# Optimization experiments

Measured on AMD Instinct MI355X. Metric: run time of the kernel, lower is better.

The kernel has to match this reference:

```python
import jax, jax.numpy as jnp
import numpy as np

D_MODEL = 512
N_HEADS = 8
HEAD_DIM = 64
INNER = N_HEADS * HEAD_DIM
PAD = 128  # flash-attention style tile padding used by the custom kernel


def setup_inputs() -> dict:
    key = jax.random.key(0)
    ks = jax.random.split(key, 5)
    B, S = 2, 2048
    scale = 0.02
    return {
        "hidden_states": jax.random.normal(ks[0], (B, S, D_MODEL), dtype=jnp.float32),
        "Wq": jax.random.normal(ks[1], (D_MODEL, INNER), dtype=jnp.float32) * scale,
        "Wk": jax.random.normal(ks[2], (D_MODEL, INNER), dtype=jnp.float32) * scale,
        "Wv": jax.random.normal(ks[3], (D_MODEL, INNER), dtype=jnp.float32) * scale,
        "Wo": jax.random.normal(ks[4], (INNER, D_MODEL), dtype=jnp.float32) * scale,
    }


def _padded_attention(q, k, v):
    """Emulates torch.ops.knl.fwd: pad seq to a multiple of PAD, run
    non-causal scaled dot-product attention masking padded keys, then
    slice back to the original length. q,k,v: [B, S, INNER]."""
    B, S, _ = q.shape
    pad_len = (-S) % PAD
    Sp = S + pad_len
    pad_cfg = ((0, 0), (0, pad_len), (0, 0))
    qp = jnp.pad(q, pad_cfg)
    kp = jnp.pad(k, pad_cfg)
    vp = jnp.pad(v, pad_cfg)
    # [B, H, Sp, hd]
    qh = qp.reshape(B, Sp, N_HEADS, HEAD_DIM).transpose(0, 2, 1, 3)
    kh = kp.reshape(B, Sp, N_HEADS, HEAD_DIM).transpose(0, 2, 1, 3)
    vh = vp.reshape(B, Sp, N_HEADS, HEAD_DIM).transpose(0, 2, 1, 3)
    scale = 1.0 / np.sqrt(HEAD_DIM).astype(np.float32)
    scores = jnp.einsum("bhqd,bhkd->bhqk", qh, kh) * scale  # [B,H,Sp,Sp]
    key_valid = jnp.arange(Sp) < S  # mask out padded keys
    scores = jnp.where(key_valid[None, None, None, :], scores, jnp.float32(-1e30))
    probs = jax.nn.softmax(scores, axis=-1)
    out = jnp.einsum("bhqk,bhkd->bhqd", probs, vh)  # [B,H,Sp,hd]
    out = out.transpose(0, 2, 1, 3).reshape(B, Sp, INNER)
    return out[:, :S, :]


def reference(hidden_states, Wq, Wk, Wv, Wo):
    q = hidden_states @ Wq
    k = hidden_states @ Wk
    v = hidden_states @ Wv
    attn = _padded_attention(q, k, v)
    return attn @ Wo
```

## Files before the change

kernel.cpp:

```cpp
#include <hip/hip_runtime.h>

using bf16 = __bf16;
using bf16x4 = __attribute__((ext_vector_type(4))) __bf16;
using bf16x8 = __attribute__((ext_vector_type(8))) __bf16;
using floatx4 = __attribute__((ext_vector_type(4))) float;
using half4 = __attribute__((ext_vector_type(4))) _Float16;
using half8 = __attribute__((ext_vector_type(8))) _Float16;

#define D_MODEL 512
#define S_LEN 2048
#define HD 64
#define NH 8
#define M_TOT 4096
#define NSPLIT 4
#define KSPAN (S_LEN / NSPLIT)
#define QSCALE 0.18033688f

__device__ __forceinline__ bf16x8 ld8(const bf16* p) {
    return *reinterpret_cast<const bf16x8*>(p);
}
__device__ __forceinline__ void gl_lds16(const bf16* g, bf16* l) {
    __builtin_amdgcn_global_load_lds(
        (const __attribute__((address_space(1))) void*)g,
        (__attribute__((address_space(3))) void*)l, 16, 0, 0);
}

__global__ __launch_bounds__(256) void prep(const float* __restrict__ w0,
                                            const float* __restrict__ w1,
                                            const float* __restrict__ w2,
                                            const float* __restrict__ w3,
                                            const float* __restrict__ X,
                                            bf16* __restrict__ WT,
                                            bf16* __restrict__ Xb) {
    int z = blockIdx.z;
    if (z == 4) {
        int i = (blockIdx.x * 256 + threadIdx.x) * 8;
        float4 a = *reinterpret_cast<const float4*>(X + i);
        float4 b = *reinterpret_cast<const float4*>(X + i + 4);
        bf16x8 o;
        o[0] = (bf16)a.x; o[1] = (bf16)a.y; o[2] = (bf16)a.z; o[3] = (bf16)a.w;
        o[4] = (bf16)b.x; o[5] = (bf16)b.y; o[6] = (bf16)b.z; o[7] = (bf16)b.w;
        *reinterpret_cast<bf16x8*>(Xb + i) = o;
        return;
    }
    if (blockIdx.x >= 256) return;
    __shared__ float t[32][33];
    const float* in = z == 0 ? w0 : z == 1 ? w1 : z == 2 ? w2 : w3;
    bf16* o = WT + (size_t)z * D_MODEL * D_MODEL;
    int x = threadIdx.x & 31;
    int y = threadIdx.x >> 5;
    int k0 = (blockIdx.x & 15) * 32, n0 = (blockIdx.x >> 4) * 32;
    for (int r = y; r < 32; r += 8) t[r][x] = in[(size_t)(k0 + r) * D_MODEL + n0 + x];
    __syncthreads();
    for (int r = y; r < 32; r += 8) o[(size_t)(n0 + r) * D_MODEL + k0 + x] = (bf16)t[x][r];
}

__global__ __launch_bounds__(256) void gemm_qkvf(const bf16* __restrict__ X,
                                                 const bf16* __restrict__ WT,
                                                 bf16* __restrict__ qk,
                                                 bf16* __restrict__ VT) {
    __shared__ __align__(16) bf16 As[2][64 * 64];
    __shared__ __align__(16) bf16 Bs[2][64 * 64];
    int lane = threadIdx.x & 63, wave = threadIdx.x >> 6;
    int l15 = lane & 15, quad = lane >> 4;
    int m0 = blockIdx.x * 64;
    int n0 = blockIdx.y * 64;
    int z = n0 >> 9;
    int h = (n0 >> 6) & 7;
    int wm = (wave & 1) * 32, wn = (wave >> 1) * 32;
    float oscale = (z == 0) ? QSCALE : 1.0f;

    int sr = lane >> 3;
    int sc = (lane & 7) ^ sr;
    const bf16* gA = X  + (size_t)(m0 + wave * 16 + sr) * D_MODEL + sc * 8;
    const bf16* gB = WT + (size_t)(n0 + wave * 16 + sr) * D_MODEL + sc * 8;
    int ldsOff = (wave * 16) * 64;
    int rx = l15 & 7;

    gl_lds16(gA, &As[0][ldsOff]);
    gl_lds16(gA + (size_t)8 * D_MODEL, &As[0][ldsOff + 8 * 64]);
    gl_lds16(gB, &Bs[0][ldsOff]);
    gl_lds16(gB + (size_t)8 * D_MODEL, &Bs[0][ldsOff + 8 * 64]);
    __syncthreads();

    floatx4 acc[2][2] = {};
    int cur = 0;
    for (int k0 = 0; k0 < D_MODEL; k0 += 64) {
        if (k0 + 64 < D_MODEL) {
            gl_lds16(gA + k0 + 64, &As[cur ^ 1][ldsOff]);
            gl_lds16(gA + (size_t)8 * D_MODEL + k0 + 64, &As[cur ^ 1][ldsOff + 8 * 64]);
            gl_lds16(gB + k0 + 64, &Bs[cur ^ 1][ldsOff]);
            gl_lds16(gB + (size_t)8 * D_MODEL + k0 + 64, &Bs[cur ^ 1][ldsOff + 8 * 64]);
        }
        bf16x8 af[2][2], bfr[2][2];
        #pragma unroll
        for (int mt = 0; mt < 2; mt++)
            #pragma unroll
            for (int kh = 0; kh < 2; kh++)
                af[mt][kh] = ld8(&As[cur][(wm + mt * 16 + l15) * 64 + (((quad + 4 * kh) ^ rx)) * 8]);
        #pragma unroll
        for (int nt = 0; nt < 2; nt++)
            #pragma unroll
            for (int kh = 0; kh < 2; kh++)
                bfr[nt][kh] = ld8(&Bs[cur][(wn + nt * 16 + l15) * 64 + (((quad + 4 * kh) ^ rx)) * 8]);
        #pragma unroll
        for (int mt = 0; mt < 2; mt++)
            #pragma unroll
            for (int nt = 0; nt < 2; nt++) {
                acc[mt][nt] = __builtin_amdgcn_mfma_f32_16x16x32_bf16(af[mt][0], bfr[nt][0], acc[mt][nt], 0, 0, 0);
                acc[mt][nt] = __builtin_amdgcn_mfma_f32_16x16x32_bf16(af[mt][1], bfr[nt][1], acc[mt][nt], 0, 0, 0);
            }
        __syncthreads();
        cur ^= 1;
    }

    if (z < 2) {
        bf16* dst = qk + (size_t)z * M_TOT * HD * NH;
        #pragma unroll
        for (int mt = 0; mt < 2; mt++)
            #pragma unroll
            for (int nt = 0; nt < 2; nt++)
                #pragma unroll
                for (int r = 0; r < 4; r++) {
                    int m = m0 + wm + mt * 16 + quad * 4 + r;
                    int n = wn + nt * 16 + l15;
                    int b = m >> 11, s = m & 2047;
                    dst[((size_t)(b * NH + h) * S_LEN + s) * HD + n] = (bf16)(acc[mt][nt][r] * oscale);
                }
    } else {
        #pragma unroll
        for (int mt = 0; mt < 2; mt++)
            #pragma unroll
            for (int nt = 0; nt < 2; nt++) {
                int m = m0 + wm + mt * 16 + quad * 4;
                int d = wn + nt * 16 + l15;
                int b = m >> 11, s = m & 2047;
                bf16x4 pk;
                pk[0] = (bf16)acc[mt][nt][0]; pk[1] = (bf16)acc[mt][nt][1];
                pk[2] = (bf16)acc[mt][nt][2]; pk[3] = (bf16)acc[mt][nt][3];
                *reinterpret_cast<bf16x4*>(&VT[((size_t)(b * NH + h) * HD + d) * S_LEN + s]) = pk;
            }
    }
}

__global__ __launch_bounds__(256, 4) void attn_split(const bf16* __restrict__ qg,
                                                     const bf16* __restrict__ kg,
                                                     const bf16* __restrict__ vt,
                                                     _Float16* __restrict__ Opart,
                                                     float* __restrict__ lsum) {
    __shared__ __align__(16) bf16 Kl[2][64 * 64];
    __shared__ __align__(16) bf16 Vl[2][64 * 64];
    int tid = threadIdx.x;
    int lane = tid & 63, wave = tid >> 6;
    int l15 = lane & 15, quad = lane >> 4;
    int bh = blockIdx.y, split = blockIdx.z;
    int q0 = blockIdx.x * 128;
    const bf16* qb = qg + (size_t)bh * S_LEN * HD;
    const bf16* kb = kg + (size_t)bh * S_LEN * HD + (size_t)split * KSPAN * HD;
    const bf16* vb = vt + (size_t)bh * HD * S_LEN + split * KSPAN;
    int qA = q0 + wave * 32 + l15;
    int qB = qA + 16;
    bf16x8 qf[2][2];
    qf[0][0] = ld8(qb + (size_t)qA * HD + quad * 8);
    qf[0][1] = ld8(qb + (size_t)qA * HD + 32 + quad * 8);
    qf[1][0] = ld8(qb + (size_t)qB * HD + quad * 8);
    qf[1][1] = ld8(qb + (size_t)qB * HD + 32 + quad * 8);
    floatx4 O[2][4] = {};
    float l_i[2] = {0.f, 0.f};

    int sr = lane >> 3;
    int sc = (lane & 7) ^ sr;
    const bf16* gK = kb + (size_t)(wave * 16 + sr) * HD + sc * 8;
    const bf16* gV = vb + (size_t)(wave * 16 + sr) * S_LEN + sc * 8;
    int ldsOff = (wave * 16) * 64;
    int rx = l15 & 7;
    int sa = ((quad & 1) << 5) + l15;
    int sb = sa + 16;
    bool himux = (quad & 2) != 0;

    gl_lds16(gK, &Kl[0][ldsOff]);
    gl_lds16(gK + (size_t)8 * HD, &Kl[0][ldsOff + 8 * 64]);
    gl_lds16(gV, &Vl[0][ldsOff]);
    gl_lds16(gV + (size_t)8 * S_LEN, &Vl[0][ldsOff + 8 * 64]);
    __syncthreads();

    int cur = 0;
    for (int kt = 0; kt < KSPAN; kt += 64) {
        if (kt + 64 < KSPAN) {
            gl_lds16(gK + (size_t)(kt + 64) * HD, &Kl[cur ^ 1][ldsOff]);
            gl_lds16(gK + (size_t)(kt + 72) * HD, &Kl[cur ^ 1][ldsOff + 8 * 64]);
            gl_lds16(gV + kt + 64, &Vl[cur ^ 1][ldsOff]);
            gl_lds16(gV + (size_t)8 * S_LEN + kt + 64, &Vl[cur ^ 1][ldsOff + 8 * 64]);
        }

        floatx4 sc4[2][4];
        #pragma unroll
        for (int nt = 0; nt < 4; nt++) {
            bf16x8 a0 = ld8(&Kl[cur][(nt * 16 + l15) * 64 + (quad ^ rx) * 8]);
            bf16x8 a1 = ld8(&Kl[cur][(nt * 16 + l15) * 64 + ((quad + 4) ^ rx) * 8]);
            #pragma unroll
            for (int s = 0; s < 2; s++) {
                floatx4 z = {};
                z = __builtin_amdgcn_mfma_f32_16x16x32_bf16(a0, qf[s][0], z, 0, 0, 0);
                z = __builtin_amdgcn_mfma_f32_16x16x32_bf16(a1, qf[s][1], z, 0, 0, 0);
                sc4[s][nt] = z;
            }
        }

        bf16x8 pb[2][2];
        #pragma unroll
        for (int s = 0; s < 2; s++) {
            int2 pq[4];
            #pragma unroll
            for (int nt = 0; nt < 4; nt++) {
                bf16x4 pk;
                #pragma unroll
                for (int r = 0; r < 4; r++) {
                    float p = exp2f(sc4[s][nt][r]);
                    l_i[s] += p;
                    pk[r] = (bf16)p;
                }
                pq[nt] = __builtin_bit_cast(int2, pk);
            }
            #pragma unroll
            for (int h2 = 0; h2 < 2; h2++) {
                int t0 = __shfl(pq[2 * h2].x,     sa, 64);
                int t1 = __shfl(pq[2 * h2].y,     sa, 64);
                int t2 = __shfl(pq[2 * h2 + 1].x, sa, 64);
                int t3 = __shfl(pq[2 * h2 + 1].y, sa, 64);
                int u0 = __shfl(pq[2 * h2].x,     sb, 64);
                int u1 = __shfl(pq[2 * h2].y,     sb, 64);
                int u2 = __shfl(pq[2 * h2 + 1].x, sb, 64);
                int u3 = __shfl(pq[2 * h2 + 1].y, sb, 64);
                int4 v;
                v.x = himux ? t2 : t0;
                v.y = himux ? t3 : t1;
                v.z = himux ? u2 : u0;
                v.w = himux ? u3 : u1;
                pb[s][h2] = __builtin_bit_cast(bf16x8, v);
            }
        }

        #pragma unroll
        for (int nt = 0; nt < 4; nt++) {
            bf16x8 v0 = ld8(&Vl[cur][(nt * 16 + l15) * 64 + (quad ^ rx) * 8]);
            bf16x8 v1 = ld8(&Vl[cur][(nt * 16 + l15) * 64 + ((quad + 4) ^ rx) * 8]);
            #pragma unroll
            for (int s = 0; s < 2; s++) {
                O[s][nt] = __builtin_amdgcn_mfma_f32_16x16x32_bf16(v0, pb[s][0], O[s][nt], 0, 0, 0);
                O[s][nt] = __builtin_amdgcn_mfma_f32_16x16x32_bf16(v1, pb[s][1], O[s][nt], 0, 0, 0);
            }
        }

        __syncthreads();
        cur ^= 1;
    }

    #pragma unroll
    for (int s = 0; s < 2; s++) {
        l_i[s] += __shfl_xor(l_i[s], 16, 64);
        l_i[s] += __shfl_xor(l_i[s], 32, 64);
        int q = (s == 0) ? qA : qB;
        size_t obase = (((size_t)(split * 16 + bh)) * S_LEN + q) * HD;
        #pragma unroll
        for (int nt = 0; nt < 4; nt++) {
            half4 hv;
            hv[0] = (_Float16)O[s][nt][0]; hv[1] = (_Float16)O[s][nt][1];
            hv[2] = (_Float16)O[s][nt][2]; hv[3] = (_Float16)O[s][nt][3];
            *reinterpret_cast<half4*>(&Opart[obase + nt * 16 + quad * 4]) = hv;
        }
        if (quad == 0)
            lsum[((size_t)(split * 16 + bh)) * S_LEN + q] = l_i[s];
    }
}

__global__ __launch_bounds__(256) void gemm_outm(const _Float16* __restrict__ Opart,
                                                 const float* __restrict__ lsum,
                                                 const bf16* __restrict__ WoT,
                                                 float* __restrict__ out) {
    __shared__ __align__(16) bf16 As[64 * 64];
    __shared__ __align__(16) bf16 Bs[64 * 64];
    __shared__ float invl[64 * 8];
    int tid = threadIdx.x;
    int lane = tid & 63, wave = tid >> 6;
    int l15 = lane & 15, quad = lane >> 4;
    int m0 = blockIdx.x * 64;
    int n0 = blockIdx.y * 64;
    int wm = (wave & 1) * 32, wn = (wave >> 1) * 32;

    for (int i = tid; i < 512; i += 256) {
        int row = i >> 3, h = i & 7;
        int mm = m0 + row;
        int b = mm >> 11, q = mm & 2047;
        float l = 0.f;
        #pragma unroll
        for (int s = 0; s < NSPLIT; s++)
            l += lsum[((size_t)(s * 16 + b * NH + h)) * S_LEN + q];
        invl[i] = 1.f / l;
    }

    int sr = lane >> 3;
    int sc = (lane & 7) ^ sr;
    const bf16* gB = WoT + (size_t)(n0 + wave * 16 + sr) * D_MODEL + sc * 8;
    bf16* ldsA = &As[(wave * 16) * 64];
    bf16* ldsB = &Bs[(wave * 16) * 64];
    int rx = l15 & 7;

    floatx4 acc[2][2] = {};
    for (int k0 = 0; k0 < D_MODEL; k0 += 64) {
        __syncthreads();
        gl_lds16(gB + k0, ldsB);
        gl_lds16(gB + (size_t)8 * D_MODEL + k0, ldsB + 8 * 64);
        int h = k0 >> 6;
        #pragma unroll
        for (int st = 0; st < 2; st++) {
            int row = wave * 16 + sr + st * 8;
            int mm = m0 + row;
            int b = mm >> 11, q = mm & 2047;
            float iv = invl[row * 8 + h];
            float a8[8] = {};
            #pragma unroll
            for (int s = 0; s < NSPLIT; s++) {
                half8 hp = *reinterpret_cast<const half8*>(
                    &Opart[(((size_t)(s * 16 + b * NH + h)) * S_LEN + q) * HD + sc * 8]);
                #pragma unroll
                for (int j = 0; j < 8; j++) a8[j] += (float)hp[j];
            }
            bf16x8 v;
            #pragma unroll
            for (int j = 0; j < 8; j++) v[j] = (bf16)(a8[j] * iv);
            *reinterpret_cast<bf16x8*>(ldsA + st * 512 + lane * 8) = v;
        }
        __syncthreads();
        bf16x8 af[2][2], bfr[2][2];
        #pragma unroll
        for (int mt = 0; mt < 2; mt++)
            #pragma unroll
            for (int kh = 0; kh < 2; kh++)
                af[mt][kh] = ld8(&As[(wm + mt * 16 + l15) * 64 + (((quad + 4 * kh) ^ rx)) * 8]);
        #pragma unroll
        for (int nt = 0; nt < 2; nt++)
            #pragma unroll
            for (int kh = 0; kh < 2; kh++)
                bfr[nt][kh] = ld8(&Bs[(wn + nt * 16 + l15) * 64 + (((quad + 4 * kh) ^ rx)) * 8]);
        #pragma unroll
        for (int mt = 0; mt < 2; mt++)
            #pragma unroll
            for (int nt = 0; nt < 2; nt++) {
                acc[mt][nt] = __builtin_amdgcn_mfma_f32_16x16x32_bf16(af[mt][0], bfr[nt][0], acc[mt][nt], 0, 0, 0);
                acc[mt][nt] = __builtin_amdgcn_mfma_f32_16x16x32_bf16(af[mt][1], bfr[nt][1], acc[mt][nt], 0, 0, 0);
            }
    }

    #pragma unroll
    for (int mt = 0; mt < 2; mt++)
        #pragma unroll
        for (int nt = 0; nt < 2; nt++)
            #pragma unroll
            for (int r = 0; r < 4; r++) {
                int m = m0 + wm + mt * 16 + quad * 4 + r;
                int n = n0 + wn + nt * 16 + l15;
                out[(size_t)m * D_MODEL + n] = acc[mt][nt][r];
            }
}

extern "C" void kernel_launch(void* const* d_in, const int* in_sizes, int n_in,
                              void* d_out, int out_size, void* d_ws, size_t ws_size,
                              hipStream_t stream) {
    const float* X  = (const float*)d_in[0];
    const float* Wq = (const float*)d_in[1];
    const float* Wk = (const float*)d_in[2];
    const float* Wv = (const float*)d_in[3];
    const float* Wo = (const float*)d_in[4];
    float* out = (float*)d_out;
    bf16* ws  = (bf16*)d_ws;

    bf16* Xb  = ws;
    bf16* WT  = Xb + (size_t)M_TOT * D_MODEL;
    bf16* qk  = WT + (size_t)4 * D_MODEL * D_MODEL;
    bf16* VT  = qk + (size_t)2 * M_TOT * D_MODEL;
    _Float16* Opart = (_Float16*)(VT + (size_t)M_TOT * D_MODEL);
    float* lbuf = (float*)(Opart + (size_t)NSPLIT * 16 * S_LEN * HD);

    prep<<<dim3(1024, 1, 5), 256, 0, stream>>>(Wq, Wk, Wv, Wo, X, WT, Xb);
    gemm_qkvf<<<dim3(64, 24), 256, 0, stream>>>(Xb, WT, qk, VT);
    attn_split<<<dim3(16, 16, NSPLIT), 256, 0, stream>>>(qk,
                                                         qk + (size_t)M_TOT * D_MODEL,
                                                         VT, Opart, lbuf);
    gemm_outm<<<dim3(64, 8), 256, 0, stream>>>(Opart, lbuf,
                                               WT + (size_t)3 * D_MODEL * D_MODEL, out);
}
```

Baseline: 133.7 us.

## Drop split-K attention; normalize in attention and double-buffer plain output GEMM

Attention no longer splits the key range four ways. Each block now walks all 2048 keys, normalizes by the row sum and writes bf16 output in [B,S,512] layout. The output projection becomes a plain GEMM that streams both operands through LDS with double buffering, replacing the split-reduction merge. This removes the fp16 partial writes, the l-sum buffers and the reduction reads, but cuts the attention grid from 1024 to 256 blocks, which lowers occupancy and parallelism on a large GPU.

```diff
diff --git a/kernel.cpp b/kernel.cpp
--- a/kernel.cpp
+++ b/kernel.cpp
@@ -4,16 +4,12 @@
 using bf16x4 = __attribute__((ext_vector_type(4))) __bf16;
 using bf16x8 = __attribute__((ext_vector_type(8))) __bf16;
 using floatx4 = __attribute__((ext_vector_type(4))) float;
-using half4 = __attribute__((ext_vector_type(4))) _Float16;
-using half8 = __attribute__((ext_vector_type(8))) _Float16;
 
 #define D_MODEL 512
 #define S_LEN 2048
 #define HD 64
 #define NH 8
 #define M_TOT 4096
-#define NSPLIT 4
-#define KSPAN (S_LEN / NSPLIT)
 #define QSCALE 0.18033688f
 
 __device__ __forceinline__ bf16x8 ld8(const bf16* p) {
@@ -143,21 +139,20 @@
     }
 }
 
-__global__ __launch_bounds__(256, 4) void attn_split(const bf16* __restrict__ qg,
-                                                     const bf16* __restrict__ kg,
-                                                     const bf16* __restrict__ vt,
-                                                     _Float16* __restrict__ Opart,
-                                                     float* __restrict__ lsum) {
+__global__ __launch_bounds__(256, 4) void attn_full(const bf16* __restrict__ qg,
+                                                    const bf16* __restrict__ kg,
+                                                    const bf16* __restrict__ vt,
+                                                    bf16* __restrict__ Ob) {
     __shared__ __align__(16) bf16 Kl[2][64 * 64];
     __shared__ __align__(16) bf16 Vl[2][64 * 64];
     int tid = threadIdx.x;
     int lane = tid & 63, wave = tid >> 6;
     int l15 = lane & 15, quad = lane >> 4;
-    int bh = blockIdx.y, split = blockIdx.z;
+    int bh = blockIdx.y;
     int q0 = blockIdx.x * 128;
     const bf16* qb = qg + (size_t)bh * S_LEN * HD;
-    const bf16* kb = kg + (size_t)bh * S_LEN * HD + (size_t)split * KSPAN * HD;
-    const bf16* vb = vt + (size_t)bh * HD * S_LEN + split * KSPAN;
+    const bf16* kb = kg + (size_t)bh * S_LEN * HD;
+    const bf16* vb = vt + (size_t)bh * HD * S_LEN;
     int qA = q0 + wave * 32 + l15;
     int qB = qA + 16;
     bf16x8 qf[2][2];
@@ -185,8 +180,8 @@
     __syncthreads();
 
     int cur = 0;
-    for (int kt = 0; kt < KSPAN; kt += 64) {
-        if (kt + 64 < KSPAN) {
+    for (int kt = 0; kt < S_LEN; kt += 64) {
+        if (kt + 64 < S_LEN) {
             gl_lds16(gK + (size_t)(kt + 64) * HD, &Kl[cur ^ 1][ldsOff]);
             gl_lds16(gK + (size_t)(kt + 72) * HD, &Kl[cur ^ 1][ldsOff + 8 * 64]);
             gl_lds16(gV + kt + 64, &Vl[cur ^ 1][ldsOff]);
@@ -256,93 +251,68 @@
         cur ^= 1;
     }
 
+    int b = bh >> 3, h = bh & 7;
     #pragma unroll
     for (int s = 0; s < 2; s++) {
         l_i[s] += __shfl_xor(l_i[s], 16, 64);
         l_i[s] += __shfl_xor(l_i[s], 32, 64);
+        float inv = 1.f / l_i[s];
         int q = (s == 0) ? qA : qB;
-        size_t obase = (((size_t)(split * 16 + bh)) * S_LEN + q) * HD;
+        size_t obase = ((size_t)(b * S_LEN + q)) * D_MODEL + h * HD;
         #pragma unroll
         for (int nt = 0; nt < 4; nt++) {
-            half4 hv;
-            hv[0] = (_Float16)O[s][nt][0]; hv[1] = (_Float16)O[s][nt][1];
-            hv[2] = (_Float16)O[s][nt][2]; hv[3] = (_Float16)O[s][nt][3];
-            *reinterpret_cast<half4*>(&Opart[obase + nt * 16 + quad * 4]) = hv;
-        }
-        if (quad == 0)
-            lsum[((size_t)(split * 16 + bh)) * S_LEN + q] = l_i[s];
-    }
-}
-
-__global__ __launch_bounds__(256) void gemm_outm(const _Float16* __restrict__ Opart,
-                                                 const float* __restrict__ lsum,
-                                                 const bf16* __restrict__ WoT,
-                                                 float* __restrict__ out) {
-    __shared__ __align__(16) bf16 As[64 * 64];
-    __shared__ __align__(16) bf16 Bs[64 * 64];
-    __shared__ float invl[64 * 8];
-    int tid = threadIdx.x;
-    int lane = tid & 63, wave = tid >> 6;
+            bf16x4 hv;
+            hv[0] = (bf16)(O[s][nt][0] * inv); hv[1] = (bf16)(O[s][nt][1] * inv);
+            hv[2] = (bf16)(O[s][nt][2] * inv); hv[3] = (bf16)(O[s][nt][3] * inv);
+            *reinterpret_cast<bf16x4*>(&Ob[obase + nt * 16 + quad * 4]) = hv;
+        }
+    }
+}
+
+__global__ __launch_bounds__(256) void gemm_out(const bf16* __restrict__ Ob,
+                                                const bf16* __restrict__ WoT,
+                                                float* __restrict__ out) {
+    __shared__ __align__(16) bf16 As[2][64 * 64];
+    __shared__ __align__(16) bf16 Bs[2][64 * 64];
+    int lane = threadIdx.x & 63, wave = threadIdx.x >> 6;
     int l15 = lane & 15, quad = lane >> 4;
     int m0 = blockIdx.x * 64;
     int n0 = blockIdx.y * 64;
     int wm = (wave & 1) * 32, wn = (wave >> 1) * 32;
 
-    for (int i = tid; i < 512; i += 256) {
-        int row = i >> 3, h = i & 7;
-        int mm = m0 + row;
-        int b = mm >> 11, q = mm & 2047;
-        float l = 0.f;
-        #pragma unroll
-        for (int s = 0; s < NSPLIT; s++)
-            l += lsum[((size_t)(s * 16 + b * NH + h)) * S_LEN + q];
-        invl[i] = 1.f / l;
-    }
-
     int sr = lane >> 3;
     int sc = (lane & 7) ^ sr;
+    const bf16* gA = Ob  + (size_t)(m0 + wave * 16 + sr) * D_MODEL + sc * 8;
     const bf16* gB = WoT + (size_t)(n0 + wave * 16 + sr) * D_MODEL + sc * 8;
-    bf16* ldsA = &As[(wave * 16) * 64];
-    bf16* ldsB = &Bs[(wave * 16) * 64];
+    int ldsOff = (wave * 16) * 64;
     int rx = l15 & 7;
 
+    gl_lds16(gA, &As[0][ldsOff]);
+    gl_lds16(gA + (size_t)8 * D_MODEL, &As[0][ldsOff + 8 * 64]);
+    gl_lds16(gB, &Bs[0][ldsOff]);
+    gl_lds16(gB + (size_t)8 * D_MODEL, &Bs[0][ldsOff + 8 * 64]);
+    __syncthreads();
+
     floatx4 acc[2][2] = {};
+    int cur = 0;
     for (int k0 = 0; k0 < D_MODEL; k0 += 64) {
-        __syncthreads();
-        gl_lds16(gB + k0, ldsB);
-        gl_lds16(gB + (size_t)8 * D_MODEL + k0, ldsB + 8 * 64);
-        int h = k0 >> 6;
-        #pragma unroll
-        for (int st = 0; st < 2; st++) {
-            int row = wave * 16 + sr + st * 8;
-            int mm = m0 + row;
-            int b = mm >> 11, q = mm & 2047;
-            float iv = invl[row * 8 + h];
-            float a8[8] = {};
-            #pragma unroll
-            for (int s = 0; s < NSPLIT; s++) {
-                half8 hp = *reinterpret_cast<const half8*>(
-                    &Opart[(((size_t)(s * 16 + b * NH + h)) * S_LEN + q) * HD + sc * 8]);
-                #pragma unroll
-                for (int j = 0; j < 8; j++) a8[j] += (float)hp[j];
-            }
-            bf16x8 v;
-            #pragma unroll
-            for (int j = 0; j < 8; j++) v[j] = (bf16)(a8[j] * iv);
-            *reinterpret_cast<bf16x8*>(ldsA + st * 512 + lane * 8) = v;
-        }
-        __syncthreads();
+        if (k0 + 64 < D_MODEL) {
+            gl_lds16(gA + k0 + 64, &As[cur ^ 1][ldsOff]);
+            gl_lds16(gA + (size_t)8 * D_MODEL + k0 + 64, &As[cur ^ 1][ldsOff + 8 * 64]);
+            gl_lds16(gB + k0 + 64, &Bs[cur ^ 1][ldsOff]);
+            gl_lds16(gB + (size_t)8 * D_MODEL + k0 + 64, &Bs[cur ^ 1][ldsOff + 8 * 64]);
+        }
         bf16x8 af[2][2], bfr[2][2];
         #pragma unroll
         for (int mt = 0; mt < 2; mt++)
             #pragma unroll
             for (int kh = 0; kh < 2; kh++)
-                af[mt][kh] = ld8(&As[(wm + mt * 16 + l15) * 64 + (((quad + 4 * kh) ^ rx)) * 8]);
+                af[mt][kh] = ld8(&As[cur][(wm + mt * 16 + l15) * 64 + (((quad + 4 * kh) ^ rx)) * 8]);
         #pragma unroll
         for (int nt = 0; nt < 2; nt++)
             #pragma unroll
             for (int kh = 0; kh < 2; kh++)
-                bfr[nt][kh] = ld8(&Bs[(wn + nt * 16 + l15) * 64 + (((quad + 4 * kh) ^ rx)) * 8]);
+                bfr[nt][kh] = ld8(&Bs[cur][(wn + nt * 16 + l15) * 64 + (((quad + 4 * kh) ^ rx)) * 8]);
         #pragma unroll
         for (int mt = 0; mt < 2; mt++)
             #pragma unroll
@@ -350,6 +320,8 @@
                 acc[mt][nt] = __builtin_amdgcn_mfma_f32_16x16x32_bf16(af[mt][0], bfr[nt][0], acc[mt][nt], 0, 0, 0);
                 acc[mt][nt] = __builtin_amdgcn_mfma_f32_16x16x32_bf16(af[mt][1], bfr[nt][1], acc[mt][nt], 0, 0, 0);
             }
+        __syncthreads();
+        cur ^= 1;
     }
 
     #pragma unroll
@@ -379,14 +351,13 @@
     bf16* WT  = Xb + (size_t)M_TOT * D_MODEL;
     bf16* qk  = WT + (size_t)4 * D_MODEL * D_MODEL;
     bf16* VT  = qk + (size_t)2 * M_TOT * D_MODEL;
-    _Float16* Opart = (_Float16*)(VT + (size_t)M_TOT * D_MODEL);
-    float* lbuf = (float*)(Opart + (size_t)NSPLIT * 16 * S_LEN * HD);
+    bf16* Ob  = VT + (size_t)M_TOT * D_MODEL;
 
     prep<<<dim3(1024, 1, 5), 256, 0, stream>>>(Wq, Wk, Wv, Wo, X, WT, Xb);
     gemm_qkvf<<<dim3(64, 24), 256, 0, stream>>>(Xb, WT, qk, VT);
-    attn_split<<<dim3(16, 16, NSPLIT), 256, 0, stream>>>(qk,
-                                                         qk + (size_t)M_TOT * D_MODEL,
-                                                         VT, Opart, lbuf);
-    gemm_outm<<<dim3(64, 8), 256, 0, stream>>>(Opart, lbuf,
-                                               WT + (size_t)3 * D_MODEL * D_MODEL, out);
-}
+    attn_full<<<dim3(16, 16), 256, 0, stream>>>(qk,
+                                                qk + (size_t)M_TOT * D_MODEL,
+                                                VT, Ob);
+    gemm_out<<<dim3(64, 8), 256, 0, stream>>>(Ob,
+                                              WT + (size_t)3 * D_MODEL * D_MODEL, out);
+}
```

Measured after the change: 148.0 us. +10.7%, slower.
